# Optimization experiments

Hardware: AMD Instinct MI355X
Metric: run time of the kernel (lower is better)

## Reference

```python
import jax, jax.numpy as jnp
import numpy as np

N_NODES = 50000


def _gcn_norm(edge_index, n):
    # add self loops, compute symmetric normalization coefficients
    src = jnp.concatenate([edge_index[0], jnp.arange(n, dtype=edge_index.dtype)])
    dst = jnp.concatenate([edge_index[1], jnp.arange(n, dtype=edge_index.dtype)])
    deg = jax.ops.segment_sum(jnp.ones_like(dst, dtype=jnp.float32), dst, num_segments=n)
    dis = jnp.where(deg > 0, jax.lax.rsqrt(jnp.maximum(deg, 1.0)), 0.0)
    norm = dis[src] * dis[dst]  # [E+n]
    return src, dst, norm


def _gcn_conv(x, W, b, src, dst, norm, n):
    xw = x @ W                      # [n, out]
    msg = xw[src] * norm[:, None]   # gather + scale
    out = jax.ops.segment_sum(msg, dst, num_segments=n)
    return out + b


def setup_inputs() -> dict:
    key = jax.random.key(0)
    ks = jax.random.split(key, 12)
    n, d, h, E, P = N_NODES, 512, 512, 400000, 200000
    sc = lambda fan_in: 1.0 / np.sqrt(fan_in)
    return {
        "x": jax.random.normal(ks[0], (n, d), dtype=jnp.float32),
        "edge_index": jax.random.randint(ks[1], (2, E), 0, n, dtype=jnp.int32),
        "edge_pairs": jax.random.randint(ks[2], (2, P), 0, n, dtype=jnp.int32),
        "W1": jax.random.uniform(ks[3], (d, h), jnp.float32, -sc(d), sc(d)),
        "b1": jnp.zeros((h,), jnp.float32),
        "W2": jax.random.uniform(ks[4], (h, h), jnp.float32, -sc(h), sc(h)),
        "b2": jnp.zeros((h,), jnp.float32),
        "lpW1": jax.random.uniform(ks[5], (2 * h, h), jnp.float32, -sc(2 * h), sc(2 * h)),
        "lpb1": jax.random.uniform(ks[6], (h,), jnp.float32, -sc(2 * h), sc(2 * h)),
        "lpW2": jax.random.uniform(ks[7], (h, 1), jnp.float32, -sc(h), sc(h)),
        "lpb2": jax.random.uniform(ks[8], (1,), jnp.float32, -sc(h), sc(h)),
    }


def reference(x, edge_index, edge_pairs, W1, b1, W2, b2, lpW1, lpb1, lpW2, lpb2):
    n = x.shape[0]
    src, dst, norm = _gcn_norm(edge_index, n)
    # encoder: GCNConv -> relu -> (dropout is identity at inference) -> GCNConv
    z = _gcn_conv(x, W1, b1, src, dst, norm, n)
    z = jax.nn.relu(z)
    z = _gcn_conv(z, W2, b2, src, dst, norm, n)
    # link predictor: gather-concat MLP
    h = jnp.concatenate([z[edge_pairs[0]], z[edge_pairs[1]]], axis=-1)  # [P, 2h]
    h = jax.nn.relu(h @ lpW1 + lpb1)
    logits = (h @ lpW2 + lpb2)[:, 0]
    return jax.nn.sigmoid(logits)
```

## Files before the change

### kernel.cpp

```cpp
#include <hip/hip_runtime.h>
#include <hip/hip_bf16.h>
#include <math.h>

#define TPB 256

typedef __attribute__((ext_vector_type(8))) short bf16x8;
typedef __attribute__((ext_vector_type(4))) float f32x4;

__device__ __forceinline__ unsigned cvt_bf(float f) {
    unsigned u = __float_as_uint(f);
    u += 0x7fffu + ((u >> 16) & 1u);
    return u >> 16;
}
__device__ __forceinline__ unsigned pack2(float a, float b) {
    return cvt_bf(a) | (cvt_bf(b) << 16);
}
__device__ __forceinline__ unsigned pack2f(float a, float b) {
    __hip_bfloat162 h = __float22bfloat162_rn(float2{a, b});
    unsigned u;
    __builtin_memcpy(&u, &h, 4);
    return u;
}

__device__ __forceinline__ void gload16(const void* g, void* l) {
    __builtin_amdgcn_global_load_lds(
        (const __attribute__((address_space(1))) void*)g,
        (__attribute__((address_space(3))) void*)l, 16, 0, 0);
}


__global__ void k_hist(const int* __restrict__ dst, int* __restrict__ cnt, int E) {
    int e = blockIdx.x * TPB + threadIdx.x;
    if (e < E) atomicAdd(&cnt[dst[e]], 1);
}

__global__ __launch_bounds__(256)
void k_scan1(const int* __restrict__ cnt, int* __restrict__ incl,
             int* __restrict__ bsum, int n) {
    __shared__ int sh[256];
    const int t = threadIdx.x;
    const int i = blockIdx.x * 256 + t;
    int v = (i < n) ? cnt[i] : 0;
    sh[t] = v;
    __syncthreads();
#pragma unroll
    for (int d = 1; d < 256; d <<= 1) {
        int u = (t >= d) ? sh[t - d] : 0;
        __syncthreads();
        sh[t] += u;
        __syncthreads();
    }
    if (i < n) incl[i] = sh[t];
    if (t == 255) bsum[blockIdx.x] = sh[255];
}

__global__ __launch_bounds__(256)
void k_scan2(int* __restrict__ bsum, int* __restrict__ boff,
             int* __restrict__ row_start, int n, int nb) {
    __shared__ int sh[256];
    const int t = threadIdx.x;
    int v = (t < nb) ? bsum[t] : 0;
    sh[t] = v;
    __syncthreads();
#pragma unroll
    for (int d = 1; d < 256; d <<= 1) {
        int u = (t >= d) ? sh[t - d] : 0;
        __syncthreads();
        sh[t] += u;
        __syncthreads();
    }
    if (t < nb) boff[t] = sh[t] - v;
    if (t == nb - 1) row_start[n] = sh[t];
}

__global__ void k_scan3(const int* __restrict__ cnt, const int* __restrict__ incl,
                        const int* __restrict__ boff, int* __restrict__ row_start,
                        int* __restrict__ cursor, float* __restrict__ dis, int n) {
    int i = blockIdx.x * TPB + threadIdx.x;
    if (i >= n) return;
    int c = cnt[i];
    int ex = boff[i >> 8] + incl[i] - c;
    row_start[i] = ex;
    cursor[i] = ex;
    dis[i] = rsqrtf((float)c + 1.0f);
}

__global__ void k_fill_csr(const int* __restrict__ src, const int* __restrict__ dst,
                           const float* __restrict__ dis, int* __restrict__ cursor,
                           int* __restrict__ csr_src, float* __restrict__ csr_nrm, int E) {
    int e = blockIdx.x * TPB + threadIdx.x;
    if (e >= E) return;
    int s = src[e], d = dst[e];
    int pos = atomicAdd(&cursor[d], 1);
    csr_src[pos] = s;
    csr_nrm[pos] = dis[s] * dis[d];
}


__global__ void k_f2bf(const float* __restrict__ in, unsigned short* __restrict__ out, int total8) {
    int i = blockIdx.x * TPB + threadIdx.x;
    if (i >= total8) return;
    float4 f0 = *(const float4*)(in + (size_t)i * 8);
    float4 f1 = *(const float4*)(in + (size_t)i * 8 + 4);
    uint4 o;
    o.x = pack2f(f0.x, f0.y); o.y = pack2f(f0.z, f0.w);
    o.z = pack2f(f1.x, f1.y); o.w = pack2f(f1.z, f1.w);
    *(uint4*)(out + (size_t)i * 8) = o;
}

__global__ void k_cvtT(const float* __restrict__ in, unsigned short* __restrict__ out, int K, int N) {
    int id = blockIdx.x * TPB + threadIdx.x;
    if (id >= K * N) return;
    int k = id / N, nn = id % N;
    out[(size_t)nn * K + k] = (unsigned short)cvt_bf(in[id]);
}

__global__ void k_cvtT_lp(const float* __restrict__ in, unsigned short* __restrict__ out) {
    int id = blockIdx.x * TPB + threadIdx.x;
    if (id >= 1024 * 512) return;
    int j = id >> 9, k = id & 511;
    float v = (j < 512) ? in[(size_t)k * 512 + j] : in[(size_t)(512 + k) * 512 + (j - 512)];
    out[id] = (unsigned short)cvt_bf(v);
}

__global__ __launch_bounds__(256)
void k_bias_lp(const float* __restrict__ lpW1, const float* __restrict__ b2,
               const float* __restrict__ lpb1, float* __restrict__ bias_big) {
    const int j = blockIdx.x * 4 + (threadIdx.x >> 6);
    if (j >= 1024) return;
    const int lane = threadIdx.x & 63;
    const int col = (j < 512) ? j : (j - 512);
    const int ro = (j < 512) ? 0 : 512;
    float s = 0.f;
#pragma unroll
    for (int it = 0; it < 8; ++it) {
        int k = lane + it * 64;
        s = fmaf(b2[k], lpW1[(size_t)(ro + k) * 512 + col], s);
    }
    s += __shfl_xor(s, 1, 64);
    s += __shfl_xor(s, 2, 64);
    s += __shfl_xor(s, 4, 64);
    s += __shfl_xor(s, 8, 64);
    s += __shfl_xor(s, 16, 64);
    s += __shfl_xor(s, 32, 64);
    if (lane == 0) bias_big[j] = s + ((j < 512) ? lpb1[j] : 0.f);
}


__device__ __forceinline__ void fma8(float* acc, uint4 u, float r) {
    acc[0] = fmaf(__uint_as_float(u.x << 16), r, acc[0]);
    acc[1] = fmaf(__uint_as_float(u.x & 0xffff0000u), r, acc[1]);
    acc[2] = fmaf(__uint_as_float(u.y << 16), r, acc[2]);
    acc[3] = fmaf(__uint_as_float(u.y & 0xffff0000u), r, acc[3]);
    acc[4] = fmaf(__uint_as_float(u.z << 16), r, acc[4]);
    acc[5] = fmaf(__uint_as_float(u.z & 0xffff0000u), r, acc[5]);
    acc[6] = fmaf(__uint_as_float(u.w << 16), r, acc[6]);
    acc[7] = fmaf(__uint_as_float(u.w & 0xffff0000u), r, acc[7]);
}

__global__ __launch_bounds__(256)
void k_agg_bf(const unsigned short* __restrict__ xin, const int* __restrict__ row_start,
              const int* __restrict__ csr_src, const float* __restrict__ csr_nrm,
              const float* __restrict__ dis, unsigned short* __restrict__ out, int n) {
    const int v = (blockIdx.x * TPB + threadIdx.x) >> 6;
    if (v >= n) return;
    const int lane = threadIdx.x & 63;
    const uint4* base = (const uint4*)xin;

    float d = dis[v]; float d2 = d * d;
    float acc[8];
    {
        uint4 u = base[(size_t)v * 64 + lane];
        acc[0] = d2 * __uint_as_float(u.x << 16);
        acc[1] = d2 * __uint_as_float(u.x & 0xffff0000u);
        acc[2] = d2 * __uint_as_float(u.y << 16);
        acc[3] = d2 * __uint_as_float(u.y & 0xffff0000u);
        acc[4] = d2 * __uint_as_float(u.z << 16);
        acc[5] = d2 * __uint_as_float(u.z & 0xffff0000u);
        acc[6] = d2 * __uint_as_float(u.w << 16);
        acc[7] = d2 * __uint_as_float(u.w & 0xffff0000u);
    }
    const int beg = row_start[v], end = row_start[v + 1];
    int j = beg;
    for (; j + 1 < end; j += 2) {
        int s0 = csr_src[j], s1 = csr_src[j + 1];
        float r0 = csr_nrm[j], r1 = csr_nrm[j + 1];
        uint4 u0 = base[(size_t)s0 * 64 + lane];
        uint4 u1 = base[(size_t)s1 * 64 + lane];
        fma8(acc, u0, r0);
        fma8(acc, u1, r1);
    }
    if (j < end) {
        uint4 u = base[(size_t)csr_src[j] * 64 + lane];
        fma8(acc, u, csr_nrm[j]);
    }
    uint4 o;
    o.x = pack2f(acc[0], acc[1]); o.y = pack2f(acc[2], acc[3]);
    o.z = pack2f(acc[4], acc[5]); o.w = pack2f(acc[6], acc[7]);
    ((uint4*)out)[(size_t)v * 64 + lane] = o;
}


__global__ __launch_bounds__(256)
void k_gemm_bf(const unsigned short* __restrict__ A, const unsigned short* __restrict__ Bt,
               const float* __restrict__ bias, unsigned short* __restrict__ C,
               int M, int K, int N, int do_relu, int nbx) {
    const int lin = blockIdx.x;
    const int xcd = lin & 7, seq = lin >> 3;
    const int rowt = xcd + 8 * (seq / nbx);
    const int colt = seq % nbx;
    const int m0 = rowt * 128;
    if (m0 >= M + 127) return;
    const int n0 = colt * 128;

    __shared__ __align__(16) char Asl[2 * 128 * 64];
    __shared__ __align__(16) char Bsl[2 * 128 * 64];
    const int t = threadIdx.x;
    const int wid = t >> 6, l = t & 63;
    const int wr = (wid >> 1) * 64, wc = (wid & 1) * 64;
    const int lrow = l & 15, g = l >> 4;

    const int srow = (l >> 2);
    const int cb_src = ((l & 3) * 16) ^ ((srow & 3) << 4);
    const int r0 = wid * 32 + srow, r1 = r0 + 16;
    const size_t rowA0 = (size_t)min(m0 + r0, M - 1) * K * 2;
    const size_t rowA1 = (size_t)min(m0 + r1, M - 1) * K * 2;
    const size_t rowB0 = (size_t)(n0 + r0) * K * 2;
    const size_t rowB1 = (size_t)(n0 + r1) * K * 2;
    const char* Ab = (const char*)A;
    const char* Bb = (const char*)Bt;
    char* ldsA0 = Asl + (wid * 32) * 64;
    char* ldsA1 = ldsA0 + 16 * 64;
    char* ldsB0 = Bsl + (wid * 32) * 64;
    char* ldsB1 = ldsB0 + 16 * 64;
    const int rd_off = (g * 16) ^ ((lrow & 3) << 4);

    f32x4 acc[4][4] = {};
    for (int k0 = 0; k0 < K; k0 += 64) {
        const size_t kf0 = (size_t)k0 * 2 + cb_src;
        const size_t kf1 = kf0 + 64;
        gload16(Ab + rowA0 + kf0, ldsA0);
        gload16(Ab + rowA1 + kf0, ldsA1);
        gload16(Ab + rowA0 + kf1, ldsA0 + 8192);
        gload16(Ab + rowA1 + kf1, ldsA1 + 8192);
        gload16(Bb + rowB0 + kf0, ldsB0);
        gload16(Bb + rowB1 + kf0, ldsB1);
        gload16(Bb + rowB0 + kf1, ldsB0 + 8192);
        gload16(Bb + rowB1 + kf1, ldsB1 + 8192);
        __syncthreads();
#pragma unroll
        for (int ks = 0; ks < 2; ++ks) {
            bf16x8 af[4], bfr[4];
#pragma unroll
            for (int i = 0; i < 4; ++i)
                af[i] = *(const bf16x8*)(Asl + ks * 8192 + (wr + i * 16 + lrow) * 64 + rd_off);
#pragma unroll
            for (int j = 0; j < 4; ++j)
                bfr[j] = *(const bf16x8*)(Bsl + ks * 8192 + (wc + j * 16 + lrow) * 64 + rd_off);
#pragma unroll
            for (int i = 0; i < 4; ++i)
#pragma unroll
                for (int j = 0; j < 4; ++j)
                    acc[i][j] = __builtin_amdgcn_mfma_f32_16x16x32_bf16(af[i], bfr[j], acc[i][j], 0, 0, 0);
        }
        __syncthreads();
    }

    float bv[4];
#pragma unroll
    for (int j = 0; j < 4; ++j) bv[j] = bias[n0 + wc + j * 16 + lrow];
    float* lws = (float*)Asl + wid * 1024;
    const int rrow = l >> 2, rcol = (l & 3) * 16;
#pragma unroll
    for (int i = 0; i < 4; ++i) {
#pragma unroll
        for (int e = 0; e < 4; ++e)
#pragma unroll
            for (int j = 0; j < 4; ++j) {
                float vv = acc[i][j][e] + bv[j];
                if (do_relu) vv = fmaxf(vv, 0.f);
                lws[(g * 4 + e) * 64 + j * 16 + lrow] = vv;
            }
        asm volatile("s_waitcnt lgkmcnt(0)" ::: "memory");
        __builtin_amdgcn_sched_barrier(0);
        const int grow = m0 + wr + i * 16 + rrow;
        float4 f0 = *(const float4*)&lws[rrow * 64 + rcol];
        float4 f1 = *(const float4*)&lws[rrow * 64 + rcol + 4];
        float4 f2 = *(const float4*)&lws[rrow * 64 + rcol + 8];
        float4 f3 = *(const float4*)&lws[rrow * 64 + rcol + 12];
        if (grow < M) {
            uint4 o0, o1;
            o0.x = pack2f(f0.x, f0.y); o0.y = pack2f(f0.z, f0.w);
            o0.z = pack2f(f1.x, f1.y); o0.w = pack2f(f1.z, f1.w);
            o1.x = pack2f(f2.x, f2.y); o1.y = pack2f(f2.z, f2.w);
            o1.z = pack2f(f3.x, f3.y); o1.w = pack2f(f3.z, f3.w);
            *(uint4*)(C + (size_t)grow * N + n0 + wc + rcol)     = o0;
            *(uint4*)(C + (size_t)grow * N + n0 + wc + rcol + 8) = o1;
        }
        asm volatile("s_waitcnt lgkmcnt(0)" ::: "memory");
        __builtin_amdgcn_sched_barrier(0);
    }
}


__global__ __launch_bounds__(256)
void k_pair(const unsigned short* __restrict__ uv, const int* __restrict__ pair, int P,
            const float* __restrict__ w2, const float* __restrict__ lpb2,
            float* __restrict__ out) {
    const int idx = (blockIdx.x * TPB + threadIdx.x) >> 6;
    if (idx >= P) return;
    const int lane = threadIdx.x & 63;
    const int p0n = pair[idx], p1n = pair[P + idx];
    const uint4 a = *(const uint4*)(uv + (size_t)p0n * 1024 + lane * 8);
    const uint4 b = *(const uint4*)(uv + (size_t)p1n * 1024 + 512 + lane * 8);
    const float4 w0 = *(const float4*)(w2 + lane * 8);
    const float4 w1 = *(const float4*)(w2 + lane * 8 + 4);
    const unsigned ua[4] = {a.x, a.y, a.z, a.w};
    const unsigned ub[4] = {b.x, b.y, b.z, b.w};
    const float wv[8] = {w0.x, w0.y, w0.z, w0.w, w1.x, w1.y, w1.z, w1.w};
    float s = 0.f;
#pragma unroll
    for (int q = 0; q < 4; ++q) {
        float h0 = __uint_as_float(ua[q] << 16) + __uint_as_float(ub[q] << 16);
        float h1 = __uint_as_float(ua[q] & 0xffff0000u) + __uint_as_float(ub[q] & 0xffff0000u);
        s = fmaf(fmaxf(h0, 0.f), wv[2 * q], s);
        s = fmaf(fmaxf(h1, 0.f), wv[2 * q + 1], s);
    }
    s += __shfl_xor(s, 1, 64);
    s += __shfl_xor(s, 2, 64);
    s += __shfl_xor(s, 4, 64);
    s += __shfl_xor(s, 8, 64);
    s += __shfl_xor(s, 16, 64);
    s += __shfl_xor(s, 32, 64);
    if (lane == 0) out[idx] = 1.0f / (1.0f + expf(-(s + lpb2[0])));
}


extern "C" void kernel_launch(void* const* d_in, const int* in_sizes, int n_in,
                              void* d_out, int out_size, void* d_ws, size_t ws_size,
                              hipStream_t stream) {
    const float* x    = (const float*)d_in[0];
    const int*   ei   = (const int*)d_in[1];
    const int*   ep   = (const int*)d_in[2];
    const float* W1   = (const float*)d_in[3];
    const float* b1   = (const float*)d_in[4];
    const float* W2   = (const float*)d_in[5];
    const float* b2   = (const float*)d_in[6];
    const float* lpW1 = (const float*)d_in[7];
    const float* lpb1 = (const float*)d_in[8];
    const float* lpW2 = (const float*)d_in[9];
    const float* lpb2 = (const float*)d_in[10];

    const int n = in_sizes[0] / 512;
    const int E = in_sizes[1] / 2;
    const int P = in_sizes[2] / 2;
    const int* src = ei;
    const int* dst = ei + E;

    char* w = (char*)d_ws;
    size_t off = 0;
    auto alloc = [&](size_t bytes) {
        void* p = w + off;
        off = (off + bytes + 255) & ~(size_t)255;
        return p;
    };
    int*   cnt       = (int*)alloc((size_t)n * 4);
    int*   incl      = (int*)alloc((size_t)n * 4);
    int*   bsum      = (int*)alloc((size_t)256 * 4);
    int*   boff      = (int*)alloc((size_t)256 * 4);
    int*   row_start = (int*)alloc((size_t)(n + 1) * 4);
    int*   cursor    = (int*)alloc((size_t)n * 4);
    int*   csr_src   = (int*)alloc((size_t)E * 4);
    float* csr_nrm   = (float*)alloc((size_t)E * 4);
    float* dis       = (float*)alloc((size_t)n * 4);
    unsigned short* w1t    = (unsigned short*)alloc((size_t)512 * 512 * 2);
    unsigned short* w2bf   = (unsigned short*)alloc((size_t)512 * 512 * 2);
    unsigned short* lpw1t  = (unsigned short*)alloc((size_t)1024 * 512 * 2);
    unsigned short* wfT    = (unsigned short*)alloc((size_t)1024 * 512 * 2);
    float* bias_big  = (float*)alloc((size_t)1024 * 4);
    float* zerob     = (float*)alloc((size_t)1024 * 4);
    unsigned short* bufA = (unsigned short*)alloc((size_t)n * 512 * 2);
    unsigned short* bufB = (unsigned short*)alloc((size_t)n * 512 * 2);
    unsigned short* uv   = (unsigned short*)alloc((size_t)n * 1024 * 2);

    dim3 blk(TPB);
    const int nb_n = (n + TPB - 1) / TPB;
    const int nb_E = (E + TPB - 1) / TPB;
    const int nb_scan = (n + 255) / 256;

    (void)hipMemsetAsync(cnt, 0, (size_t)n * 4, stream);
    (void)hipMemsetAsync(zerob, 0, (size_t)1024 * 4, stream);
    k_hist<<<nb_E, blk, 0, stream>>>(dst, cnt, E);
    k_scan1<<<nb_scan, 256, 0, stream>>>(cnt, incl, bsum, n);
    k_scan2<<<1, 256, 0, stream>>>(bsum, boff, row_start, n, nb_scan);
    k_scan3<<<nb_n, blk, 0, stream>>>(cnt, incl, boff, row_start, cursor, dis, n);
    k_fill_csr<<<nb_E, blk, 0, stream>>>(src, dst, dis, cursor, csr_src, csr_nrm, E);

    k_f2bf<<<(n * 64 + TPB - 1) / TPB, blk, 0, stream>>>(x, bufA, n * 64);
    k_cvtT<<<(512 * 512 + TPB - 1) / TPB, blk, 0, stream>>>(W1, w1t, 512, 512);
    k_f2bf<<<(512 * 64 + TPB - 1) / TPB, blk, 0, stream>>>(W2, w2bf, 512 * 64);
    k_cvtT_lp<<<(1024 * 512 + TPB - 1) / TPB, blk, 0, stream>>>(lpW1, lpw1t);
    k_bias_lp<<<256, blk, 0, stream>>>(lpW1, b2, lpb1, bias_big);

    const int gy  = (n + 127) / 128;
    const int gy8 = ((gy + 7) / 8) * 8;
    const int agg_blocks = (n * 64 + TPB - 1) / TPB;

    k_gemm_bf<<<4 * 8, blk, 0, stream>>>(lpw1t, w2bf, zerob, wfT, 1024, 512, 512, 0, 4);

    k_agg_bf<<<agg_blocks, blk, 0, stream>>>(bufA, row_start, csr_src, csr_nrm, dis, bufB, n);
    k_gemm_bf<<<4 * gy8, blk, 0, stream>>>(bufB, w1t, b1, bufA, n, 512, 512, 1, 4);
    k_agg_bf<<<agg_blocks, blk, 0, stream>>>(bufA, row_start, csr_src, csr_nrm, dis, bufB, n);
    k_gemm_bf<<<8 * gy8, blk, 0, stream>>>(bufB, wfT, bias_big, uv, n, 512, 1024, 0, 8);

    k_pair<<<(P * 64 + TPB - 1) / TPB, blk, 0, stream>>>(uv, ep, P, lpW2, lpb2, (float*)d_out);
}
```

Measured before the change: 442.3 us.

## Add 256x256 triple-buffered pipelined GEMM for the big node GEMMs

Adds a new 512-thread GEMM kernel with 256x256 output tiles, a three-stage LDS ring with prefetch two K-steps ahead, vmcnt-based waits and raised wave priority around the MFMA blocks. The two large node-level GEMMs now use it, which should hide global-load latency and improve data reuse per tile. The old 128x128 GEMM is reduced to 32-wide K steps with direct per-element stores and is kept only for the small weight-fusion GEMM. The aggregation loop is also unrolled to four neighbours per step for more memory-level parallelism. The new kernel needs 96KB of dynamic LDS and many accumulator registers, which may limit occupancy.

```diff
diff --git a/kernel.cpp b/kernel.cpp
--- a/kernel.cpp
+++ b/kernel.cpp
@@ -11,9 +11,6 @@
     unsigned u = __float_as_uint(f);
     u += 0x7fffu + ((u >> 16) & 1u);
     return u >> 16;
-}
-__device__ __forceinline__ unsigned pack2(float a, float b) {
-    return cvt_bf(a) | (cvt_bf(b) << 16);
 }
 __device__ __forceinline__ unsigned pack2f(float a, float b) {
     __hip_bfloat162 h = __float22bfloat162_rn(float2{a, b});
@@ -182,15 +179,21 @@
     }
     const int beg = row_start[v], end = row_start[v + 1];
     int j = beg;
-    for (; j + 1 < end; j += 2) {
+    for (; j + 3 < end; j += 4) {
         int s0 = csr_src[j], s1 = csr_src[j + 1];
+        int s2 = csr_src[j + 2], s3 = csr_src[j + 3];
         float r0 = csr_nrm[j], r1 = csr_nrm[j + 1];
+        float r2 = csr_nrm[j + 2], r3 = csr_nrm[j + 3];
         uint4 u0 = base[(size_t)s0 * 64 + lane];
         uint4 u1 = base[(size_t)s1 * 64 + lane];
+        uint4 u2 = base[(size_t)s2 * 64 + lane];
+        uint4 u3 = base[(size_t)s3 * 64 + lane];
         fma8(acc, u0, r0);
         fma8(acc, u1, r1);
-    }
-    if (j < end) {
+        fma8(acc, u2, r2);
+        fma8(acc, u3, r3);
+    }
+    for (; j < end; ++j) {
         uint4 u = base[(size_t)csr_src[j] * 64 + lane];
         fma8(acc, u, csr_nrm[j]);
     }
@@ -213,8 +216,8 @@
     if (m0 >= M + 127) return;
     const int n0 = colt * 128;
 
-    __shared__ __align__(16) char Asl[2 * 128 * 64];
-    __shared__ __align__(16) char Bsl[2 * 128 * 64];
+    __shared__ __align__(16) char Asl[128 * 64];
+    __shared__ __align__(16) char Bsl[128 * 64];
     const int t = threadIdx.x;
     const int wid = t >> 6, l = t & 63;
     const int wr = (wid >> 1) * 64, wc = (wid & 1) * 64;
@@ -236,43 +239,140 @@
     const int rd_off = (g * 16) ^ ((lrow & 3) << 4);
 
     f32x4 acc[4][4] = {};
-    for (int k0 = 0; k0 < K; k0 += 64) {
-        const size_t kf0 = (size_t)k0 * 2 + cb_src;
-        const size_t kf1 = kf0 + 64;
-        gload16(Ab + rowA0 + kf0, ldsA0);
-        gload16(Ab + rowA1 + kf0, ldsA1);
-        gload16(Ab + rowA0 + kf1, ldsA0 + 8192);
-        gload16(Ab + rowA1 + kf1, ldsA1 + 8192);
-        gload16(Bb + rowB0 + kf0, ldsB0);
-        gload16(Bb + rowB1 + kf0, ldsB1);
-        gload16(Bb + rowB0 + kf1, ldsB0 + 8192);
-        gload16(Bb + rowB1 + kf1, ldsB1 + 8192);
+    for (int k0 = 0; k0 < K; k0 += 32) {
+        const size_t koff = (size_t)k0 * 2 + cb_src;
+        gload16(Ab + rowA0 + koff, ldsA0);
+        gload16(Ab + rowA1 + koff, ldsA1);
+        gload16(Bb + rowB0 + koff, ldsB0);
+        gload16(Bb + rowB1 + koff, ldsB1);
         __syncthreads();
-#pragma unroll
-        for (int ks = 0; ks < 2; ++ks) {
-            bf16x8 af[4], bfr[4];
+        bf16x8 af[4], bfr[4];
+#pragma unroll
+        for (int i = 0; i < 4; ++i)
+            af[i] = *(const bf16x8*)(Asl + (wr + i * 16 + lrow) * 64 + rd_off);
+#pragma unroll
+        for (int j = 0; j < 4; ++j)
+            bfr[j] = *(const bf16x8*)(Bsl + (wc + j * 16 + lrow) * 64 + rd_off);
+#pragma unroll
+        for (int i = 0; i < 4; ++i)
+#pragma unroll
+            for (int j = 0; j < 4; ++j)
+                acc[i][j] = __builtin_amdgcn_mfma_f32_16x16x32_bf16(af[i], bfr[j], acc[i][j], 0, 0, 0);
+        __syncthreads();
+    }
+    float bv[4];
+#pragma unroll
+    for (int j = 0; j < 4; ++j) bv[j] = bias[n0 + wc + j * 16 + lrow];
+#pragma unroll
+    for (int i = 0; i < 4; ++i) {
+        const int rb = m0 + wr + i * 16 + g * 4;
+#pragma unroll
+        for (int e = 0; e < 4; ++e) {
+            const int row = rb + e;
+            if (row < M) {
+#pragma unroll
+                for (int j = 0; j < 4; ++j) {
+                    float vv = acc[i][j][e] + bv[j];
+                    if (do_relu) vv = fmaxf(vv, 0.f);
+                    C[(size_t)row * N + n0 + wc + j * 16 + lrow] = (unsigned short)cvt_bf(vv);
+                }
+            }
+        }
+    }
+}
+
+
+__global__ __launch_bounds__(512, 2)
+void k_gemm256(const unsigned short* __restrict__ A, const unsigned short* __restrict__ Bt,
+               const float* __restrict__ bias, unsigned short* __restrict__ C,
+               int M, int K, int N, int do_relu, int nbx) {
+    const int lin = blockIdx.x;
+    const int xcd = lin & 7, seq = lin >> 3;
+    const int rowt = xcd + 8 * (seq / nbx);
+    const int colt = seq % nbx;
+    const int m0 = rowt * 256;
+    if (m0 >= M) return;
+    const int n0 = colt * 256;
+
+    extern __shared__ __align__(16) char lds[];
+    char* ldsA = lds;
+    char* ldsB = lds + 3 * 16384;
+
+    const int t = threadIdx.x;
+    const int wid = t >> 6, l = t & 63;
+    const int wm = wid >> 2, wn = wid & 3;
+    const int lrow = l & 15, g = l >> 4;
+
+    const int sr = l & 15, sc = l >> 4;
+    const size_t K2 = (size_t)K * 2;
+    const size_t aA0 = (size_t)min(m0 + wid * 32 + sr, M - 1) * K2 + sc * 16;
+    const size_t aA1 = (size_t)min(m0 + wid * 32 + 16 + sr, M - 1) * K2 + sc * 16;
+    const size_t aB0 = (size_t)(n0 + wid * 32 + sr) * K2 + sc * 16;
+    const size_t aB1 = aB0 + (size_t)16 * K2;
+    const char* Ag = (const char*)A;
+    const char* Bg = (const char*)Bt;
+
+    const int nt = K >> 5;
+    f32x4 acc[8][4] = {};
+
+#define STAGE(tt, q) do {                                                    \
+        const int _b = (tt) % 3;                                             \
+        if ((q) == 0) gload16(Ag + aA0 + (size_t)(tt) * 64,                  \
+                              ldsA + _b * 16384 + (2 * wid) * 1024);         \
+        if ((q) == 1) gload16(Ag + aA1 + (size_t)(tt) * 64,                  \
+                              ldsA + _b * 16384 + (2 * wid + 1) * 1024);     \
+        if ((q) == 2) gload16(Bg + aB0 + (size_t)(tt) * 64,                  \
+                              ldsB + _b * 16384 + (2 * wid) * 1024);         \
+        if ((q) == 3) gload16(Bg + aB1 + (size_t)(tt) * 64,                  \
+                              ldsB + _b * 16384 + (2 * wid + 1) * 1024);     \
+    } while (0)
+
+#pragma unroll
+    for (int q = 0; q < 4; ++q) STAGE(0, q);
+#pragma unroll
+    for (int q = 0; q < 4; ++q) STAGE(1, q);
+    asm volatile("s_waitcnt vmcnt(4)" ::: "memory");
+    __builtin_amdgcn_s_barrier();
+    __builtin_amdgcn_sched_barrier(0);
+
+    for (int tt = 0; tt < nt; ++tt) {
+        const char* Abl = ldsA + (tt % 3) * 16384 + (wm * 8) * 1024 + g * 256 + lrow * 16;
+        const char* Bbl = ldsB + (tt % 3) * 16384 + (wn * 4) * 1024 + g * 256 + lrow * 16;
+        const bool pf = (tt + 2 < nt);
+#pragma unroll
+        for (int q = 0; q < 4; ++q) {
+            if (pf) STAGE(tt + 2, q);
+            const int mb = (q >> 1) * 4, nb = (q & 1) * 2;
+            bf16x8 af[4], bfr[2];
 #pragma unroll
             for (int i = 0; i < 4; ++i)
-                af[i] = *(const bf16x8*)(Asl + ks * 8192 + (wr + i * 16 + lrow) * 64 + rd_off);
-#pragma unroll
-            for (int j = 0; j < 4; ++j)
-                bfr[j] = *(const bf16x8*)(Bsl + ks * 8192 + (wc + j * 16 + lrow) * 64 + rd_off);
+                af[i] = *(const bf16x8*)(Abl + (mb + i) * 1024);
+#pragma unroll
+            for (int j = 0; j < 2; ++j)
+                bfr[j] = *(const bf16x8*)(Bbl + (nb + j) * 1024);
+            __builtin_amdgcn_s_setprio(1);
 #pragma unroll
             for (int i = 0; i < 4; ++i)
 #pragma unroll
-                for (int j = 0; j < 4; ++j)
-                    acc[i][j] = __builtin_amdgcn_mfma_f32_16x16x32_bf16(af[i], bfr[j], acc[i][j], 0, 0, 0);
+                for (int j = 0; j < 2; ++j)
+                    acc[mb + i][nb + j] = __builtin_amdgcn_mfma_f32_16x16x32_bf16(
+                        af[i], bfr[j], acc[mb + i][nb + j], 0, 0, 0);
+            __builtin_amdgcn_s_setprio(0);
         }
-        __syncthreads();
-    }
+        if (pf) asm volatile("s_waitcnt vmcnt(4)" ::: "memory");
+        else    asm volatile("s_waitcnt vmcnt(0)" ::: "memory");
+        __builtin_amdgcn_s_barrier();
+        __builtin_amdgcn_sched_barrier(0);
+    }
+#undef STAGE
 
     float bv[4];
 #pragma unroll
-    for (int j = 0; j < 4; ++j) bv[j] = bias[n0 + wc + j * 16 + lrow];
-    float* lws = (float*)Asl + wid * 1024;
+    for (int j = 0; j < 4; ++j) bv[j] = bias[n0 + wn * 64 + j * 16 + lrow];
+    float* lws = (float*)(lds + wid * 4096);
     const int rrow = l >> 2, rcol = (l & 3) * 16;
 #pragma unroll
-    for (int i = 0; i < 4; ++i) {
+    for (int i = 0; i < 8; ++i) {
 #pragma unroll
         for (int e = 0; e < 4; ++e)
 #pragma unroll
@@ -283,7 +383,7 @@
             }
         asm volatile("s_waitcnt lgkmcnt(0)" ::: "memory");
         __builtin_amdgcn_sched_barrier(0);
-        const int grow = m0 + wr + i * 16 + rrow;
+        const int grow = m0 + wm * 128 + i * 16 + rrow;
         float4 f0 = *(const float4*)&lws[rrow * 64 + rcol];
         float4 f1 = *(const float4*)&lws[rrow * 64 + rcol + 4];
         float4 f2 = *(const float4*)&lws[rrow * 64 + rcol + 8];
@@ -294,8 +394,8 @@
             o0.z = pack2f(f1.x, f1.y); o0.w = pack2f(f1.z, f1.w);
             o1.x = pack2f(f2.x, f2.y); o1.y = pack2f(f2.z, f2.w);
             o1.z = pack2f(f3.x, f3.y); o1.w = pack2f(f3.z, f3.w);
-            *(uint4*)(C + (size_t)grow * N + n0 + wc + rcol)     = o0;
-            *(uint4*)(C + (size_t)grow * N + n0 + wc + rcol + 8) = o1;
+            *(uint4*)(C + (size_t)grow * N + n0 + wn * 64 + rcol)     = o0;
+            *(uint4*)(C + (size_t)grow * N + n0 + wn * 64 + rcol + 8) = o1;
         }
         asm volatile("s_waitcnt lgkmcnt(0)" ::: "memory");
         __builtin_amdgcn_sched_barrier(0);
@@ -402,16 +502,16 @@
     k_cvtT_lp<<<(1024 * 512 + TPB - 1) / TPB, blk, 0, stream>>>(lpW1, lpw1t);
     k_bias_lp<<<256, blk, 0, stream>>>(lpW1, b2, lpb1, bias_big);
 
-    const int gy  = (n + 127) / 128;
-    const int gy8 = ((gy + 7) / 8) * 8;
     const int agg_blocks = (n * 64 + TPB - 1) / TPB;
+    const int gy256  = (n + 255) / 256;
+    const int gy256p = ((gy256 + 7) / 8) * 8;
 
     k_gemm_bf<<<4 * 8, blk, 0, stream>>>(lpw1t, w2bf, zerob, wfT, 1024, 512, 512, 0, 4);
 
     k_agg_bf<<<agg_blocks, blk, 0, stream>>>(bufA, row_start, csr_src, csr_nrm, dis, bufB, n);
-    k_gemm_bf<<<4 * gy8, blk, 0, stream>>>(bufB, w1t, b1, bufA, n, 512, 512, 1, 4);
+    k_gemm256<<<2 * gy256p, dim3(512), 98304, stream>>>(bufB, w1t, b1, bufA, n, 512, 512, 1, 2);
     k_agg_bf<<<agg_blocks, blk, 0, stream>>>(bufA, row_start, csr_src, csr_nrm, dis, bufB, n);
-    k_gemm_bf<<<8 * gy8, blk, 0, stream>>>(bufB, wfT, bias_big, uv, n, 512, 1024, 0, 8);
+    k_gemm256<<<4 * gy256p, dim3(512), 98304, stream>>>(bufB, wfT, bias_big, uv, n, 512, 1024, 0, 4);
 
     k_pair<<<(P * 64 + TPB - 1) / TPB, blk, 0, stream>>>(uv, ep, P, lpW2, lpb2, (float*)d_out);
 }
```

Measured after the change: 443.4 us. Within noise of the previous version (+0.3%).
